# Performance work log

Hardware: AMD Instinct MI355X
Metric: run time of the kernel (lower is better)

The kernel has to match this reference:

```python
import jax, jax.numpy as jnp
import numpy as np

GROUP_SIZE = 64
M, K, N, RANK = 4096, 4096, 4096, 32


def setup_inputs() -> dict:
    key = jax.random.key(0)
    ks = jax.random.split(key, 7)
    x = jax.random.normal(ks[0], (M, K), dtype=jnp.float32)
    # int4 weight residual in [-8, 7]
    q_w = jax.random.randint(ks[1], (K, N), -8, 8, dtype=jnp.int32)
    # positive per-group weight scales, shape (K // group_size, N)
    wscales = jax.random.uniform(ks[2], (K // GROUP_SIZE, N), dtype=jnp.float32) * 0.01 + 1e-4
    lora_down = jax.random.normal(ks[3], (K, RANK), dtype=jnp.float32) * 0.02
    lora_up = jax.random.normal(ks[4], (RANK, N), dtype=jnp.float32) * 0.02
    # smoothing factors, strictly positive
    smooth = jax.random.uniform(ks[5], (K,), dtype=jnp.float32) + 0.5
    bias = jax.random.normal(ks[6], (N,), dtype=jnp.float32)
    return {"x": x, "q_w": q_w, "wscales": wscales, "lora_down": lora_down,
            "lora_up": lora_up, "smooth": smooth, "bias": bias}


def reference(x, q_w, wscales, lora_down, lora_up, smooth, bias):
    G = GROUP_SIZE
    m, k = x.shape
    n = q_w.shape[1]
    ng = k // G  # groups along K

    # smooth activation: move outliers into weights
    x_smooth = x / smooth[None, :]

    # per-group symmetric int4 quantize + dequantize of activations
    xg = x_smooth.reshape(m, ng, G)
    ascales = jnp.maximum(jnp.max(jnp.abs(xg), axis=-1) / 7.0, 1e-8)  # (m, ng)
    qx = jnp.clip(jnp.round(xg / ascales[..., None]), -8.0, 7.0)
    x_dq = (qx * ascales[..., None]).reshape(m, k)

    # dequantize int4 weight residual: grouped along K
    W_dq = (q_w.astype(jnp.float32).reshape(ng, G, n) * wscales[:, None, :]).reshape(k, n)

    # simulated int4 GEMM + fp LoRA residual + bias
    y_main = x_dq @ W_dq
    y_lora = (x @ lora_down) @ lora_up
    return y_main + y_lora + bias[None, :]
```

## Files before the change

kernel.cpp:

```cpp
#include <hip/hip_runtime.h>
#include <hip/hip_bf16.h>
#include <stdint.h>

#define GSIZE 64
#define MDIM 4096
#define KDIM 4096
#define NDIM 4096
#define RANK 32
#define KE   4160
#define NG   64
#define NSPLIT 8

#define N_LORATQ 256
#define N_WPREP  (65 * 64)
#define NBLOCKS  (N_LORATQ + N_WPREP)

typedef __bf16 bf16x4 __attribute__((ext_vector_type(4)));
typedef __bf16 bf16x8 __attribute__((ext_vector_type(8)));
typedef float  f32x4  __attribute__((ext_vector_type(4)));

#define GPTR(p) ((__attribute__((address_space(1))) void*)(uintptr_t)(p))
#define LPTR(p) ((__attribute__((address_space(3))) void*)(p))

__global__ __launch_bounds__(512) void k_prep(const float* __restrict__ x,
                                              const int*   __restrict__ qw,
                                              const float* __restrict__ wsc,
                                              const float* __restrict__ ld,
                                              const float* __restrict__ lu,
                                              const float* __restrict__ smooth,
                                              __bf16* __restrict__ A,
                                              __bf16* __restrict__ Wt,
                                              float* __restrict__ tws) {
    __shared__ __attribute__((aligned(16))) char smem[10240];
    int b   = blockIdx.x;
    int tid = threadIdx.x;

    if (b < N_LORATQ) {
        int m0    = (b & 31) * 128;
        int sp    = b >> 5;
        int kbase = sp * 512;

        {
            int c4 = tid & 127;
            int r0 = tid >> 7;
            float4 sv = *(const float4*)(smooth + kbase + c4 * 4);
            float4 si = {__builtin_amdgcn_rcpf(sv.x), __builtin_amdgcn_rcpf(sv.y),
                         __builtin_amdgcn_rcpf(sv.z), __builtin_amdgcn_rcpf(sv.w)};
            #pragma unroll 4
            for (int p = 0; p < 32; ++p) {
                int row = r0 + p * 4;
                float4 xv = *(const float4*)(x + (size_t)(m0 + row) * KDIM + kbase + c4 * 4);
                float4 xs = {xv.x * si.x, xv.y * si.y, xv.z * si.z, xv.w * si.w};
                float a = fmaxf(fmaxf(fabsf(xs.x), fabsf(xs.y)),
                                fmaxf(fabsf(xs.z), fabsf(xs.w)));
                #pragma unroll
                for (int off = 1; off < 16; off <<= 1)
                    a = fmaxf(a, __shfl_xor(a, off, 64));
                float ascale = fmaxf(a * (1.0f / 7.0f), 1e-8f);
                float rin = __builtin_amdgcn_rcpf(ascale);
                float q0 = fminf(fmaxf(rintf(xs.x * rin), -8.f), 7.f);
                float q1 = fminf(fmaxf(rintf(xs.y * rin), -8.f), 7.f);
                float q2 = fminf(fmaxf(rintf(xs.z * rin), -8.f), 7.f);
                float q3 = fminf(fmaxf(rintf(xs.w * rin), -8.f), 7.f);
                bf16x4 av = {(__bf16)(q0 * ascale), (__bf16)(q1 * ascale),
                             (__bf16)(q2 * ascale), (__bf16)(q3 * ascale)};
                *(bf16x4*)(A + (size_t)(m0 + row) * KE + kbase + c4 * 4) = av;
            }
        }

        __bf16* AsL = (__bf16*)smem;
        __bf16* BsL = (__bf16*)(smem + 8192);
        int lane = tid & 63;
        int wave = tid >> 6;
        int quad = lane >> 4;
        int mrow = lane & 15;

        f32x4 z = {0.f, 0.f, 0.f, 0.f};
        f32x4 acc[2];
        acc[0] = z; acc[1] = z;

        for (int step = 0; step < 16; ++step) {
            int kk = kbase + step * 32;
            {
                int slot = tid;
                int r = slot >> 2;
                int g = (slot & 3) ^ (r & 3);
                const float* src = x + (size_t)(m0 + r) * KDIM + kk + g * 8;
                float4 a0 = *(const float4*)src;
                float4 a1 = *(const float4*)(src + 4);
                bf16x8 v = {(__bf16)a0.x, (__bf16)a0.y, (__bf16)a0.z, (__bf16)a0.w,
                            (__bf16)a1.x, (__bf16)a1.y, (__bf16)a1.z, (__bf16)a1.w};
                *(bf16x8*)(AsL + slot * 8) = v;
            }
            #pragma unroll
            for (int i2 = 0; i2 < 2; ++i2) {
                int j = i2 * 512 + tid;
                int r = j >> 5, n = j & 31;
                BsL[n * 32 + r] = (__bf16)ld[(size_t)(kk + r) * RANK + n];
            }
            __syncthreads();
            bf16x8 av, bv[2];
            {
                int row  = wave * 16 + mrow;
                int slot = row * 4 + (quad ^ (row & 3));
                av = *(const bf16x8*)(AsL + slot * 8);
            }
            #pragma unroll
            for (int j = 0; j < 2; ++j)
                bv[j] = *(const bf16x8*)(BsL + (j * 16 + mrow) * 32 + quad * 8);
            #pragma unroll
            for (int j = 0; j < 2; ++j)
                acc[j] = __builtin_amdgcn_mfma_f32_16x16x32_bf16(av, bv[j], acc[j], 0, 0, 0);
            __syncthreads();
        }
        float* tout = tws + (size_t)sp * MDIM * RANK;
        #pragma unroll
        for (int j = 0; j < 2; ++j)
            #pragma unroll
            for (int r = 0; r < 4; ++r) {
                int rowg = m0 + wave * 16 + quad * 4 + r;
                int col  = j * 16 + mrow;
                tout[(size_t)rowg * RANK + col] = acc[j][r];
            }
        return;
    }

    {
        __bf16 (*tile)[68] = (__bf16(*)[68])smem;
        int widx = b - N_LORATQ;
        int n0 = (widx & 63) * 64;
        int kt = widx >> 6;
        int k0 = kt * 64;
        int tr = tid >> 4;
        int tc = (tid & 15) * 4;
        if (kt < NG) {
            float4 ws = *(const float4*)(wsc + (size_t)kt * NDIM + n0 + tc);
            #pragma unroll
            for (int r = tr; r < 64; r += 32) {
                int4 q = *(const int4*)(qw + (size_t)(k0 + r) * NDIM + n0 + tc);
                tile[r][tc + 0] = (__bf16)((float)q.x * ws.x);
                tile[r][tc + 1] = (__bf16)((float)q.y * ws.y);
                tile[r][tc + 2] = (__bf16)((float)q.z * ws.z);
                tile[r][tc + 3] = (__bf16)((float)q.w * ws.w);
            }
        } else {
            #pragma unroll
            for (int r = tr; r < 64; r += 32) {
                if (r < RANK) {
                    float4 lv = *(const float4*)(lu + (size_t)r * NDIM + n0 + tc);
                    tile[r][tc + 0] = (__bf16)lv.x;
                    tile[r][tc + 1] = (__bf16)lv.y;
                    tile[r][tc + 2] = (__bf16)lv.z;
                    tile[r][tc + 3] = (__bf16)lv.w;
                } else {
                    tile[r][tc + 0] = (__bf16)0.f;
                    tile[r][tc + 1] = (__bf16)0.f;
                    tile[r][tc + 2] = (__bf16)0.f;
                    tile[r][tc + 3] = (__bf16)0.f;
                }
            }
        }
        __syncthreads();
        int nn = tid >> 3;
        int ks = (tid & 7) * 8;
        bf16x8 v;
        #pragma unroll
        for (int e = 0; e < 8; ++e) v[e] = tile[ks + e][nn];
        *(bf16x8*)(Wt + (size_t)(n0 + nn) * KE + k0 + ks) = v;
    }
}

__global__ __launch_bounds__(256) void k_fin(const float* __restrict__ tws,
                                             __bf16* __restrict__ A) {
    int idx = blockIdx.x * 256 + threadIdx.x;
    int m = idx >> 4, cq = idx & 15;
    int c = cq * 4;
    bf16x4 v = {(__bf16)0.f, (__bf16)0.f, (__bf16)0.f, (__bf16)0.f};
    if (c < RANK) {
        f32x4 s = {0.f, 0.f, 0.f, 0.f};
        #pragma unroll
        for (int sp = 0; sp < NSPLIT; ++sp) {
            f32x4 p = *(const f32x4*)(tws + ((size_t)sp * MDIM + m) * RANK + c);
            s.x += p.x; s.y += p.y; s.z += p.z; s.w += p.w;
        }
        v[0] = (__bf16)s.x; v[1] = (__bf16)s.y; v[2] = (__bf16)s.z; v[3] = (__bf16)s.w;
    }
    *(bf16x4*)(A + (size_t)m * KE + KDIM + c) = v;
}

#define NT (KE / 64)
#define HS 8192
#define BS 16384

#define STAGE(ldsbase, gb, kt, half) do {                                     \
    int _k0 = (kt) * 64;                                                      \
    _Pragma("unroll")                                                         \
    for (int _it = 0; _it < 2; ++_it) {                                       \
        int _c = _it * 512 + tid;                                             \
        int _r = _c >> 3;                                                     \
        int _g = (_c & 7) ^ (_r & 7);                                         \
        __builtin_amdgcn_global_load_lds(                                     \
            GPTR((gb) + (size_t)((half) * 128 + _r) * KE + _k0 + _g * 8),     \
            LPTR((char*)(ldsbase) + (_it * 512 + wave * 64) * 16),            \
            16, 0, 0);                                                        \
    } } while (0)

#define RD_A(dst, base, qm) do {                                              \
    _Pragma("unroll")                                                         \
    for (int _i = 0; _i < 4; ++_i) {                                          \
        int _row = (qm) * 128 + wm * 64 + _i * 16 + mrow;                     \
        dst[0][_i] = *(const bf16x8*)((const char*)(base) + _row * 128 + ga0 * 16); \
        dst[1][_i] = *(const bf16x8*)((const char*)(base) + _row * 128 + ga1 * 16); \
    } } while (0)

#define RD_B(dst, base, qn) do {                                              \
    _Pragma("unroll")                                                         \
    for (int _j = 0; _j < 2; ++_j) {                                          \
        int _row = (qn) * 128 + wn * 32 + _j * 16 + mrow;                     \
        dst[0][_j] = *(const bf16x8*)((const char*)(base) + _row * 128 + ga0 * 16); \
        dst[1][_j] = *(const bf16x8*)((const char*)(base) + _row * 128 + ga1 * 16); \
    } } while (0)

#define MMA(qm, qn, AV, BV) do {                                              \
    _Pragma("unroll")                                                         \
    for (int _i = 0; _i < 4; ++_i)                                            \
        _Pragma("unroll")                                                     \
        for (int _j = 0; _j < 2; ++_j) {                                      \
            acc[qm][qn][_i][_j] = __builtin_amdgcn_mfma_f32_16x16x32_bf16(    \
                AV[0][_i], BV[0][_j], acc[qm][qn][_i][_j], 0, 0, 0);          \
            acc[qm][qn][_i][_j] = __builtin_amdgcn_mfma_f32_16x16x32_bf16(    \
                AV[1][_i], BV[1][_j], acc[qm][qn][_i][_j], 0, 0, 0);          \
        } } while (0)

#define SBAR0() __builtin_amdgcn_sched_barrier(0)

__global__ __launch_bounds__(512, 2) void k_gemm(const __bf16* __restrict__ A,
                                                 const __bf16* __restrict__ Wt,
                                                 const float*  __restrict__ bias,
                                                 float* __restrict__ out) {
    __shared__ __attribute__((aligned(16))) __bf16 As[2 * BS];
    __shared__ __attribute__((aligned(16))) __bf16 Bs[2 * BS];
    int tid  = threadIdx.x;
    int lane = tid & 63;
    int wave = tid >> 6;
    int quad = lane >> 4;
    int mrow = lane & 15;
    int wm = wave >> 2;
    int wn = wave & 3;

    int lin = blockIdx.y * 16 + blockIdx.x;
    int swz = (lin & 7) * 32 + (lin >> 3);
    int m0 = (swz >> 4) * 256, n0 = (swz & 15) * 256;

    const __bf16* Ab = A  + (size_t)m0 * KE;
    const __bf16* Bb = Wt + (size_t)n0 * KE;

    int ga0 = quad ^ (mrow & 7);
    int ga1 = (quad + 4) ^ (mrow & 7);

    f32x4 z = {0.f, 0.f, 0.f, 0.f};
    f32x4 acc[2][2][4][2];
    #pragma unroll
    for (int a = 0; a < 2; ++a)
        #pragma unroll
        for (int b = 0; b < 2; ++b)
            #pragma unroll
            for (int i = 0; i < 4; ++i)
                #pragma unroll
                for (int j = 0; j < 2; ++j) acc[a][b][i][j] = z;

    STAGE(As,           Ab, 0, 0);
    STAGE(Bs + HS,      Bb, 0, 1);
    STAGE(Bs,           Bb, 0, 0);
    STAGE(As + HS,      Ab, 0, 1);
    STAGE(As + BS,      Ab, 1, 0);
    STAGE(Bs + BS + HS, Bb, 1, 1);
    asm volatile("s_waitcnt vmcnt(4)" ::: "memory");
    __builtin_amdgcn_s_barrier();
    SBAR0();

    bf16x8 av0[2][4], av1[2][4], bv0[2][2], bv1[2][2];
    RD_A(av0, As, 0);
    RD_B(bv0, Bs, 0);
    SBAR0();

    for (int t = 0; t < NT; ++t) {
        int cur = t & 1;
        const __bf16* Acur = As + cur * BS;
        const __bf16* Bcur = Bs + cur * BS;
        __bf16* Anx = As + (cur ^ 1) * BS;
        __bf16* Bnx = Bs + (cur ^ 1) * BS;
        __bf16* Acu = As + cur * BS;
        __bf16* Bcu = Bs + cur * BS;
        bool s1 = (t + 1 < NT), s2 = (t + 2 < NT);

        if (s1) STAGE(Bnx, Bb, t + 1, 0);
        RD_B(bv1, Bcur, 1);
        SBAR0();
        asm volatile("s_waitcnt lgkmcnt(4)" ::: "memory");
        SBAR0();
        __builtin_amdgcn_s_setprio(1);
        MMA(0, 0, av0, bv0);
        __builtin_amdgcn_s_setprio(0);

        if (s1) STAGE(Anx + HS, Ab, t + 1, 1);
        RD_A(av1, Acur, 1);
        SBAR0();
        asm volatile("s_waitcnt lgkmcnt(8)" ::: "memory");
        SBAR0();
        __builtin_amdgcn_s_setprio(1);
        MMA(0, 1, av0, bv1);
        __builtin_amdgcn_s_setprio(0);
        __builtin_amdgcn_s_barrier();
        SBAR0();

        if (s2) STAGE(Acu, Ab, t + 2, 0);
        SBAR0();
        asm volatile("s_waitcnt lgkmcnt(0)" ::: "memory");
        SBAR0();
        __builtin_amdgcn_s_setprio(1);
        MMA(1, 1, av1, bv1);
        __builtin_amdgcn_s_setprio(0);
        if (s2) { asm volatile("s_waitcnt vmcnt(2)" ::: "memory"); }
        else    { asm volatile("s_waitcnt vmcnt(0)" ::: "memory"); }
        __builtin_amdgcn_s_barrier();
        SBAR0();

        if (s2) STAGE(Bcu + HS, Bb, t + 2, 1);
        if (s1) RD_A(av0, Anx, 0);
        SBAR0();
        __builtin_amdgcn_s_setprio(1);
        MMA(1, 0, av1, bv0);
        __builtin_amdgcn_s_setprio(0);
        if (s1) RD_B(bv0, Bnx, 0);
        SBAR0();
    }

    #pragma unroll
    for (int qn = 0; qn < 2; ++qn)
        #pragma unroll
        for (int j = 0; j < 2; ++j) {
            int col = n0 + qn * 128 + wn * 32 + j * 16 + mrow;
            float bvs = bias[col];
            #pragma unroll
            for (int qm = 0; qm < 2; ++qm)
                #pragma unroll
                for (int i = 0; i < 4; ++i) {
                    int rbase = m0 + qm * 128 + wm * 64 + i * 16 + quad * 4;
                    #pragma unroll
                    for (int r = 0; r < 4; ++r)
                        __builtin_nontemporal_store(acc[qm][qn][i][j][r] + bvs,
                                                    &out[(size_t)(rbase + r) * NDIM + col]);
                }
        }
}

extern "C" void kernel_launch(void* const* d_in, const int* in_sizes, int n_in,
                              void* d_out, int out_size, void* d_ws, size_t ws_size,
                              hipStream_t stream) {
    const float* x    = (const float*)d_in[0];
    const int*   qw   = (const int*)  d_in[1];
    const float* wsc  = (const float*)d_in[2];
    const float* ld   = (const float*)d_in[3];
    const float* lu   = (const float*)d_in[4];
    const float* sm   = (const float*)d_in[5];
    const float* bias = (const float*)d_in[6];
    float* out = (float*)d_out;

    char* ws = (char*)d_ws;
    __bf16* A   = (__bf16*)ws;
    __bf16* Wt  = (__bf16*)(ws + (size_t)MDIM * KE * 2);
    float*  tws = (float*) (ws + (size_t)MDIM * KE * 4);

    k_prep<<<NBLOCKS, 512, 0, stream>>>(x, qw, wsc, ld, lu, sm, A, Wt, tws);
    k_fin<<<(MDIM * 16) / 256, 256, 0, stream>>>(tws, A);
    k_gemm<<<dim3(NDIM / 256, MDIM / 256), 512, 0, stream>>>(A, Wt, bias, out);
}
```

Before: 306.5 us.

## Fuse activation quantization with LoRA-down x staging in shared memory

The LoRA-down blocks now read x once per 256-column chunk. In the same pass they write the quantized activations and a bf16 copy of x into a swizzled 64KB LDS buffer, and the lora_down MFMA loop then runs over that buffer. Before, x was read twice, once for quantization and once per 32-wide k step for the MFMA. The change also cuts the number of barriers per block and changes the weight-prep tile padding from 68 to 65. The larger 80KB static LDS allocation applies to every block of the kernel, including the weight-prep blocks, which can reduce occupancy.

```diff
diff --git a/kernel.cpp b/kernel.cpp
--- a/kernel.cpp
+++ b/kernel.cpp
@@ -31,88 +31,85 @@
                                               __bf16* __restrict__ A,
                                               __bf16* __restrict__ Wt,
                                               float* __restrict__ tws) {
-    __shared__ __attribute__((aligned(16))) char smem[10240];
+    __shared__ __attribute__((aligned(16))) char smem[81920];
     int b   = blockIdx.x;
     int tid = threadIdx.x;
 
     if (b < N_LORATQ) {
-        int m0    = (b & 31) * 128;
-        int sp    = b >> 5;
-        int kbase = sp * 512;
-
-        {
-            int c4 = tid & 127;
-            int r0 = tid >> 7;
-            float4 sv = *(const float4*)(smooth + kbase + c4 * 4);
-            float4 si = {__builtin_amdgcn_rcpf(sv.x), __builtin_amdgcn_rcpf(sv.y),
-                         __builtin_amdgcn_rcpf(sv.z), __builtin_amdgcn_rcpf(sv.w)};
-            #pragma unroll 4
-            for (int p = 0; p < 32; ++p) {
-                int row = r0 + p * 4;
-                float4 xv = *(const float4*)(x + (size_t)(m0 + row) * KDIM + kbase + c4 * 4);
-                float4 xs = {xv.x * si.x, xv.y * si.y, xv.z * si.z, xv.w * si.w};
-                float a = fmaxf(fmaxf(fabsf(xs.x), fabsf(xs.y)),
-                                fmaxf(fabsf(xs.z), fabsf(xs.w)));
-                #pragma unroll
-                for (int off = 1; off < 16; off <<= 1)
-                    a = fmaxf(a, __shfl_xor(a, off, 64));
-                float ascale = fmaxf(a * (1.0f / 7.0f), 1e-8f);
-                float rin = __builtin_amdgcn_rcpf(ascale);
-                float q0 = fminf(fmaxf(rintf(xs.x * rin), -8.f), 7.f);
-                float q1 = fminf(fmaxf(rintf(xs.y * rin), -8.f), 7.f);
-                float q2 = fminf(fmaxf(rintf(xs.z * rin), -8.f), 7.f);
-                float q3 = fminf(fmaxf(rintf(xs.w * rin), -8.f), 7.f);
-                bf16x4 av = {(__bf16)(q0 * ascale), (__bf16)(q1 * ascale),
-                             (__bf16)(q2 * ascale), (__bf16)(q3 * ascale)};
-                *(bf16x4*)(A + (size_t)(m0 + row) * KE + kbase + c4 * 4) = av;
-            }
-        }
-
-        __bf16* AsL = (__bf16*)smem;
-        __bf16* BsL = (__bf16*)(smem + 8192);
+        __bf16* Xs  = (__bf16*)smem;
+        __bf16* BsL = (__bf16*)(smem + 65536);
+        int m0 = (b & 31) * 128;
+        int sp = b >> 5;
         int lane = tid & 63;
         int wave = tid >> 6;
         int quad = lane >> 4;
         int mrow = lane & 15;
+        int c4   = tid & 63;
 
         f32x4 z = {0.f, 0.f, 0.f, 0.f};
         f32x4 acc[2];
         acc[0] = z; acc[1] = z;
 
-        for (int step = 0; step < 16; ++step) {
-            int kk = kbase + step * 32;
+        #pragma unroll
+        for (int sub = 0; sub < 2; ++sub) {
+            int kb = sp * 512 + sub * 256;
+
+            #pragma unroll
+            for (int i = 0; i < 16; ++i) {
+                int idx = i * 512 + tid;
+                int k = idx >> 5, n = idx & 31;
+                *(__bf16*)((char*)BsL + n * 512 +
+                           ((((k >> 3) ^ (n & 7)) << 4) | ((k & 7) << 1)))
+                    = (__bf16)ld[(size_t)(kb + k) * RANK + n];
+            }
+
             {
-                int slot = tid;
-                int r = slot >> 2;
-                int g = (slot & 3) ^ (r & 3);
-                const float* src = x + (size_t)(m0 + r) * KDIM + kk + g * 8;
-                float4 a0 = *(const float4*)src;
-                float4 a1 = *(const float4*)(src + 4);
-                bf16x8 v = {(__bf16)a0.x, (__bf16)a0.y, (__bf16)a0.z, (__bf16)a0.w,
-                            (__bf16)a1.x, (__bf16)a1.y, (__bf16)a1.z, (__bf16)a1.w};
-                *(bf16x8*)(AsL + slot * 8) = v;
-            }
-            #pragma unroll
-            for (int i2 = 0; i2 < 2; ++i2) {
-                int j = i2 * 512 + tid;
-                int r = j >> 5, n = j & 31;
-                BsL[n * 32 + r] = (__bf16)ld[(size_t)(kk + r) * RANK + n];
+                float4 sv = *(const float4*)(smooth + kb + c4 * 4);
+                float4 si = {__builtin_amdgcn_rcpf(sv.x), __builtin_amdgcn_rcpf(sv.y),
+                             __builtin_amdgcn_rcpf(sv.z), __builtin_amdgcn_rcpf(sv.w)};
+                int g = c4 >> 1;
+                #pragma unroll 4
+                for (int p = 0; p < 16; ++p) {
+                    int row = wave + 8 * p;
+                    float4 xv = *(const float4*)(x + (size_t)(m0 + row) * KDIM + kb + c4 * 4);
+                    float4 xs = {xv.x * si.x, xv.y * si.y, xv.z * si.z, xv.w * si.w};
+                    float a = fmaxf(fmaxf(fabsf(xs.x), fabsf(xs.y)),
+                                    fmaxf(fabsf(xs.z), fabsf(xs.w)));
+                    #pragma unroll
+                    for (int off = 1; off < 16; off <<= 1)
+                        a = fmaxf(a, __shfl_xor(a, off, 64));
+                    float ascale = fmaxf(a * (1.0f / 7.0f), 1e-8f);
+                    float rin = __builtin_amdgcn_rcpf(ascale);
+                    float q0 = fminf(fmaxf(rintf(xs.x * rin), -8.f), 7.f);
+                    float q1 = fminf(fmaxf(rintf(xs.y * rin), -8.f), 7.f);
+                    float q2 = fminf(fmaxf(rintf(xs.z * rin), -8.f), 7.f);
+                    float q3 = fminf(fmaxf(rintf(xs.w * rin), -8.f), 7.f);
+                    bf16x4 aq = {(__bf16)(q0 * ascale), (__bf16)(q1 * ascale),
+                                 (__bf16)(q2 * ascale), (__bf16)(q3 * ascale)};
+                    *(bf16x4*)(A + (size_t)(m0 + row) * KE + kb + c4 * 4) = aq;
+                    bf16x4 xb = {(__bf16)xv.x, (__bf16)xv.y, (__bf16)xv.z, (__bf16)xv.w};
+                    *(bf16x4*)((char*)Xs + row * 512 +
+                               (((g ^ (row & 7)) << 4) | ((c4 & 1) << 3))) = xb;
+                }
             }
             __syncthreads();
-            bf16x8 av, bv[2];
-            {
-                int row  = wave * 16 + mrow;
-                int slot = row * 4 + (quad ^ (row & 3));
-                av = *(const bf16x8*)(AsL + slot * 8);
-            }
-            #pragma unroll
-            for (int j = 0; j < 2; ++j)
-                bv[j] = *(const bf16x8*)(BsL + (j * 16 + mrow) * 32 + quad * 8);
-            #pragma unroll
-            for (int j = 0; j < 2; ++j)
-                acc[j] = __builtin_amdgcn_mfma_f32_16x16x32_bf16(av, bv[j], acc[j], 0, 0, 0);
+
+            #pragma unroll
+            for (int step = 0; step < 8; ++step) {
+                int row = wave * 16 + mrow;
+                bf16x8 av = *(const bf16x8*)((char*)Xs + row * 512 +
+                                             (((step * 4 + quad) ^ (row & 7)) << 4));
+                #pragma unroll
+                for (int j = 0; j < 2; ++j) {
+                    int n = j * 16 + mrow;
+                    bf16x8 bv = *(const bf16x8*)((char*)BsL + n * 512 +
+                                                 (((step * 4 + quad) ^ (n & 7)) << 4));
+                    acc[j] = __builtin_amdgcn_mfma_f32_16x16x32_bf16(av, bv, acc[j], 0, 0, 0);
+                }
+            }
             __syncthreads();
         }
+
         float* tout = tws + (size_t)sp * MDIM * RANK;
         #pragma unroll
         for (int j = 0; j < 2; ++j)
@@ -126,7 +123,7 @@
     }
 
     {
-        __bf16 (*tile)[68] = (__bf16(*)[68])smem;
+        __bf16 (*tile)[65] = (__bf16(*)[65])smem;
         int widx = b - N_LORATQ;
         int n0 = (widx & 63) * 64;
         int kt = widx >> 6;
```

Measured after the change: 309.6 us. Within noise of the previous version (+1.0%).
